# Performance work log

Measured on AMD Instinct MI355X. Metric: run time of the kernel, lower is better.

Reference implementation:

```python
import math
import jax, jax.numpy as jnp
import numpy as np

THETA = 10000.0

def _rotate_half(x):
    # lucidrains interleaved pairs: (d r) with r=2
    x = x.reshape(*x.shape[:-1], -1, 2)
    x1, x2 = x[..., 0], x[..., 1]
    return jnp.stack([-x2, x1], axis=-1).reshape(*x.shape[:-2], -1)

def _apply_rotary(x):
    # x: [B, H, S, D]
    seq_len, d = x.shape[-2], x.shape[-1]
    inv_freq = 1.0 / (THETA ** (jnp.arange(0, d, 2, dtype=jnp.float32) / d))  # [D/2]
    t = jnp.arange(seq_len, dtype=jnp.float32)
    freqs = t[:, None] * inv_freq[None, :]                 # [S, D/2]
    freqs = jnp.repeat(freqs, 2, axis=-1)                  # [S, D] interleaved
    cos, sin = jnp.cos(freqs), jnp.sin(freqs)
    return x * cos + _rotate_half(x) * sin

def setup_inputs() -> dict:
    key = jax.random.key(0)
    k1, k2, k3, k4 = jax.random.split(key, 4)
    B, H, S, D = 2, 16, 2048, 64
    q = jax.random.normal(k1, (B, H, S, D), dtype=jnp.float32)
    k = jax.random.normal(k2, (B, H, S, D), dtype=jnp.float32)
    v = jax.random.normal(k3, (B, H, S, D), dtype=jnp.float32)
    mask = jax.random.randint(k4, (B, 1, S, S), 0, 2, dtype=jnp.int32)
    return {"q": q, "k": k, "v": v, "mask": mask}

def reference(q, k, v, mask):
    d = k.shape[-1]
    qr = _apply_rotary(q)
    kr = _apply_rotary(k)
    score = jnp.einsum('bhqd,bhkd->bhqk', qr, kr) / math.sqrt(d)
    score = jnp.where(mask == 0, jnp.float32(-10000.0), score)
    score = jax.nn.softmax(score, axis=-1)
    out = jnp.einsum('bhqk,bhkd->bhqd', score, v)
    return (out, score)
```

## Files before the change

### kernel.cpp

```cpp
#include <hip/hip_runtime.h>
#include <hip/hip_fp16.h>

#define NB 2
#define NH 16
#define NS 2048
#define ND 64

typedef __attribute__((ext_vector_type(8))) _Float16 half8;
typedef __attribute__((ext_vector_type(4))) _Float16 half4;
typedef __attribute__((ext_vector_type(4))) float float4v;

static constexpr int NE = NB * NH * NS * ND;
static constexpr int TPB = 512;

__device__ __forceinline__ void wg_barrier_lds() {
    asm volatile("s_waitcnt lgkmcnt(0)" ::: "memory");
    __builtin_amdgcn_s_barrier();
    __builtin_amdgcn_sched_barrier(0);
}

static constexpr int ROPE_BLKS = (NE / 2) / 256;
static constexpr int VT_BLKS   = NE / 256;
static constexpr int MP_BLKS   = (NB * NS * NS) / 256;

__global__ void prep_kernel(const float* __restrict__ q,
                            const float* __restrict__ k,
                            const float* __restrict__ v,
                            const int* __restrict__ mask,
                            _Float16* __restrict__ qr,
                            _Float16* __restrict__ kr6,
                            _Float16* __restrict__ v4,
                            unsigned int* __restrict__ mp) {
    int blk = blockIdx.x;
    if (blk < ROPE_BLKS) {
        int idx = blk * 256 + threadIdx.x;
        int i   = idx & 31;
        int row = idx >> 5;
        int s   = row & (NS - 1);
        int bh  = row >> 11;

        float inv_freq = expf((float)i * -0.2878231366242710f);
        float ang = (float)s * inv_freq;
        float sn, cs;
        sincosf(ang, &sn, &cs);

        size_t base = (size_t)row * ND + 2 * i;
        float q0 = q[base], q1 = q[base + 1];
        float k0 = k[base], k1 = k[base + 1];
        qr[base]     = (_Float16)(q0 * cs - q1 * sn);
        qr[base + 1] = (_Float16)(q1 * cs + q0 * sn);

        int oct = i >> 2;
        int j0  = (2 * i) & 7;
        size_t t6 = ((size_t)(bh * 128 + (s >> 4)) * 8 + oct) * 128 + (s & 15) * 8 + j0;
        kr6[t6]     = (_Float16)(k0 * cs - k1 * sn);
        kr6[t6 + 1] = (_Float16)(k1 * cs + k0 * sn);
    } else if (blk < ROPE_BLKS + VT_BLKS) {
        int idx = (blk - ROPE_BLKS) * 256 + threadIdx.x;
        int j    = idx & 3;
        int lm   = (idx >> 2) & 15;
        int kq   = (idx >> 6) & 3;
        int dblk = (idx >> 8) & 3;
        int kt   = (idx >> 10) & 127;
        int bh   = idx >> 17;
        int key  = kt * 16 + kq * 4 + j;
        int d    = dblk * 16 + lm;
        v4[idx] = (_Float16)v[((size_t)bh * NS + key) * ND + d];
    } else {
        size_t idx = (size_t)(blk - ROPE_BLKS - VT_BLKS) * 256 + threadIdx.x;
        unsigned long long bal = __ballot(mask[idx] != 0);
        int l = threadIdx.x & 63;
        if (l == 0)       mp[idx >> 5] = (unsigned int)bal;
        else if (l == 32) mp[idx >> 5] = (unsigned int)(bal >> 32);
    }
}

static constexpr int TPH    = 264;
static constexpr int WSLICE = 16 * TPH;

__global__ __launch_bounds__(TPB, 4)
void attn_reg_kernel(const _Float16* __restrict__ qr,
                     const _Float16* __restrict__ kr6,
                     const _Float16* __restrict__ v4,
                     const unsigned int* __restrict__ mp,
                     float* __restrict__ out,
                     float* __restrict__ score) {
    __shared__ unsigned int maskb[16 * 64];
    __shared__ float        sums8[8][16];
    __shared__ _Float16     pool[8 * WSLICE];

    int wgid = (blockIdx.x & 7) * 512 + (blockIdx.x >> 3);
    int qt = wgid & 127;
    int bh = wgid >> 7;
    int b  = bh >> 4;
    int q0 = qt * 16;

    int tid = threadIdx.x;
    int w   = tid >> 6;
    int l   = tid & 63;
    int lm  = l & 15;
    int lp  = l >> 4;

    {
        const unsigned int* mrow = mp + ((size_t)b * NS + q0) * 64;
        for (int i = tid; i < 16 * 64; i += TPB) maskb[i] = mrow[i];
    }

    const _Float16* qrow = qr + ((size_t)bh * NS + q0 + lm) * ND;
    half8 a0 = *(const half8*)(qrow + lp * 8);
    half8 a1 = *(const half8*)(qrow + 32 + lp * 8);
    const _Float16* k6 = kr6 + (size_t)bh * 128 * 1024;
    _Float16* tw = pool + w * WSLICE;
    wg_barrier_lds();

    float4v ac0 = {0.f, 0.f, 0.f, 0.f};
    float4v ac1 = {0.f, 0.f, 0.f, 0.f};
    float4v ac2 = {0.f, 0.f, 0.f, 0.f};
    float4v ac3 = {0.f, 0.f, 0.f, 0.f};
    const _Float16* vb = v4 + (size_t)bh * 128 * 1024 + l * 4;
    float ps = 0.0f;
#pragma unroll
    for (int t = 0; t < 16; ++t) {
        int kt = w * 16 + t;
        const _Float16* kp = k6 + (size_t)kt * 1024 + l * 8;
        half8 b0 = *(const half8*)(kp);
        half8 b1 = *(const half8*)(kp + 512);
        float4v acc = {0.f, 0.f, 0.f, 0.f};
        acc = __builtin_amdgcn_mfma_f32_16x16x32_f16(b0, a0, acc, 0, 0, 0);
        acc = __builtin_amdgcn_mfma_f32_16x16x32_f16(b1, a1, acc, 0, 0, 0);
        int keyb = kt * 16 + lp * 4;
        unsigned int mw = maskb[lm * 64 + (keyb >> 5)];
        int bit0 = keyb & 31;
        half4 ep;
#pragma unroll
        for (int r = 0; r < 4; ++r) {
            float ev = ((mw >> (bit0 + r)) & 1u) ? __expf(acc[r] * 0.125f) : 0.0f;
            ps += ev;
            ep[r] = (_Float16)ev;
        }
        *(half4*)(tw + lm * TPH + t * 16 + lp * 4) = ep;

        const _Float16* vp = vb + (size_t)kt * 1024;
        half4 af0 = *(const half4*)(vp);
        half4 af1 = *(const half4*)(vp + 256);
        half4 af2 = *(const half4*)(vp + 512);
        half4 af3 = *(const half4*)(vp + 768);
        __builtin_amdgcn_s_setprio(1);
        ac0 = __builtin_amdgcn_mfma_f32_16x16x16f16(af0, ep, ac0, 0, 0, 0);
        ac1 = __builtin_amdgcn_mfma_f32_16x16x16f16(af1, ep, ac1, 0, 0, 0);
        ac2 = __builtin_amdgcn_mfma_f32_16x16x16f16(af2, ep, ac2, 0, 0, 0);
        ac3 = __builtin_amdgcn_mfma_f32_16x16x16f16(af3, ep, ac3, 0, 0, 0);
        __builtin_amdgcn_s_setprio(0);
    }
    ps += __shfl_xor(ps, 16);
    ps += __shfl_xor(ps, 32);
    if (lp == 0) sums8[w][lm] = ps;
    wg_barrier_lds();

    {
        float s = 0.0f;
#pragma unroll
        for (int ww = 0; ww < 8; ++ww) s += sums8[ww][lm];
        float iv = (s > 0.0f) ? (1.0f / s) : 0.0f;
        float* sbase = score + ((size_t)bh * NS + q0) * NS + w * 256;
#pragma unroll
        for (int r = 0; r < 16; ++r) {
            float ivr = __shfl(iv, r);
            half4 hv = *(const half4*)(tw + r * TPH + l * 4);
            float4v f;
            f[0] = (float)hv[0] * ivr;
            f[1] = (float)hv[1] * ivr;
            f[2] = (float)hv[2] * ivr;
            f[3] = (float)hv[3] * ivr;
            *(float4v*)(sbase + (size_t)r * NS + l * 4) = f;
        }
    }
    asm volatile("s_waitcnt lgkmcnt(0)" ::: "memory");
    __builtin_amdgcn_sched_barrier(0);

    {
        float* ow = (float*)tw + lm * 64 + lp * 4;
#pragma unroll
        for (int r = 0; r < 4; ++r) {
            ow[ 0 + r] = ac0[r];
            ow[16 + r] = ac1[r];
            ow[32 + r] = ac2[r];
            ow[48 + r] = ac3[r];
        }
    }
    wg_barrier_lds();

    {
        float* orow = out + ((size_t)bh * NS + q0) * ND;
        for (int i = tid; i < 16 * 64; i += TPB) {
            int r = i >> 6;
            float s = 0.0f;
#pragma unroll
            for (int ww = 0; ww < 8; ++ww) s += sums8[ww][r];
            float iv = (s > 0.0f) ? (1.0f / s) : 0.0f;
            float acc = 0.0f;
#pragma unroll
            for (int ww = 0; ww < 8; ++ww)
                acc += ((const float*)(pool + ww * WSLICE))[i];
            __builtin_nontemporal_store(acc * iv, &orow[i]);
        }
    }
}

extern "C" void kernel_launch(void* const* d_in, const int* in_sizes, int n_in,
                              void* d_out, int out_size, void* d_ws, size_t ws_size,
                              hipStream_t stream) {
    const float* q    = (const float*)d_in[0];
    const float* k    = (const float*)d_in[1];
    const float* v    = (const float*)d_in[2];
    const int*   mask = (const int*)d_in[3];

    float* out   = (float*)d_out;
    float* score = out + (size_t)NE;

    _Float16* qrw = (_Float16*)d_ws;
    _Float16* kr6 = qrw + NE;
    _Float16* v4w = kr6 + NE;
    unsigned int* mp = (unsigned int*)(v4w + NE);

    prep_kernel<<<dim3(ROPE_BLKS + VT_BLKS + MP_BLKS), dim3(256), 0, stream>>>(
        q, k, v, mask, qrw, kr6, v4w, mp);
    attn_reg_kernel<<<dim3(NB * NH * (NS / 16)), dim3(TPB), 0, stream>>>(
        qrw, kr6, v4w, mp, out, score);
}
```

Measured before the change: 208.7 us.

## Halve per-wave LDS staging by holding half the P tile in registers

Each wave now stages only the first 8 key tiles of exp-scores in LDS, and keeps the last 8 in registers. The score output is written in two passes: the second half is copied back into the freed LDS slice before it is normalised and stored. This halves the LDS pool so more workgroups can fit per CU, and the launch bound is raised from 4 to 6 to match. Score writes also switch to nontemporal float2 stores. The risks are extra VGPR pressure from the held tiles under the tighter register budget, which could spill, and narrower stores to global memory.

```diff
diff --git a/kernel.cpp b/kernel.cpp
--- a/kernel.cpp
+++ b/kernel.cpp
@@ -9,13 +9,18 @@
 typedef __attribute__((ext_vector_type(8))) _Float16 half8;
 typedef __attribute__((ext_vector_type(4))) _Float16 half4;
 typedef __attribute__((ext_vector_type(4))) float float4v;
-
-static constexpr int NE = NB * NH * NS * ND;
+typedef __attribute__((ext_vector_type(2))) float float2v;
+
+static constexpr int NE  = NB * NH * NS * ND;
 static constexpr int TPB = 512;
 
 __device__ __forceinline__ void wg_barrier_lds() {
     asm volatile("s_waitcnt lgkmcnt(0)" ::: "memory");
     __builtin_amdgcn_s_barrier();
+    __builtin_amdgcn_sched_barrier(0);
+}
+__device__ __forceinline__ void wave_lds_guard() {
+    asm volatile("s_waitcnt lgkmcnt(0)" ::: "memory");
     __builtin_amdgcn_sched_barrier(0);
 }
 
@@ -75,10 +80,10 @@
     }
 }
 
-static constexpr int TPH    = 264;
+static constexpr int TPH    = 136;
 static constexpr int WSLICE = 16 * TPH;
 
-__global__ __launch_bounds__(TPB, 4)
+__global__ __launch_bounds__(TPB, 6)
 void attn_reg_kernel(const _Float16* __restrict__ qr,
                      const _Float16* __restrict__ kr6,
                      const _Float16* __restrict__ v4,
@@ -110,6 +115,7 @@
     half8 a0 = *(const half8*)(qrow + lp * 8);
     half8 a1 = *(const half8*)(qrow + 32 + lp * 8);
     const _Float16* k6 = kr6 + (size_t)bh * 128 * 1024;
+    const _Float16* vb = v4 + (size_t)bh * 128 * 1024 + l * 4;
     _Float16* tw = pool + w * WSLICE;
     wg_barrier_lds();
 
@@ -117,7 +123,7 @@
     float4v ac1 = {0.f, 0.f, 0.f, 0.f};
     float4v ac2 = {0.f, 0.f, 0.f, 0.f};
     float4v ac3 = {0.f, 0.f, 0.f, 0.f};
-    const _Float16* vb = v4 + (size_t)bh * 128 * 1024 + l * 4;
+    half4 earr[8];
     float ps = 0.0f;
 #pragma unroll
     for (int t = 0; t < 16; ++t) {
@@ -138,8 +144,11 @@
             ps += ev;
             ep[r] = (_Float16)ev;
         }
-        *(half4*)(tw + lm * TPH + t * 16 + lp * 4) = ep;
-
+        if (t < 8) {
+            *(half4*)(tw + lm * TPH + t * 16 + lp * 4) = ep;
+        } else {
+            earr[t - 8] = ep;
+        }
         const _Float16* vp = vb + (size_t)kt * 1024;
         half4 af0 = *(const half4*)(vp);
         half4 af1 = *(const half4*)(vp + 256);
@@ -163,21 +172,34 @@
         for (int ww = 0; ww < 8; ++ww) s += sums8[ww][lm];
         float iv = (s > 0.0f) ? (1.0f / s) : 0.0f;
         float* sbase = score + ((size_t)bh * NS + q0) * NS + w * 256;
+
 #pragma unroll
         for (int r = 0; r < 16; ++r) {
             float ivr = __shfl(iv, r);
-            half4 hv = *(const half4*)(tw + r * TPH + l * 4);
-            float4v f;
-            f[0] = (float)hv[0] * ivr;
-            f[1] = (float)hv[1] * ivr;
-            f[2] = (float)hv[2] * ivr;
-            f[3] = (float)hv[3] * ivr;
-            *(float4v*)(sbase + (size_t)r * NS + l * 4) = f;
-        }
-    }
-    asm volatile("s_waitcnt lgkmcnt(0)" ::: "memory");
-    __builtin_amdgcn_sched_barrier(0);
-
+            half res0 = tw[r * TPH + l * 2];
+            half res1 = tw[r * TPH + l * 2 + 1];
+            float2v f;
+            f[0] = (float)(_Float16)res0 * ivr;
+            f[1] = (float)(_Float16)res1 * ivr;
+            __builtin_nontemporal_store(f, (float2v*)(sbase + (size_t)r * NS + l * 2));
+        }
+        wave_lds_guard();
+#pragma unroll
+        for (int t = 0; t < 8; ++t)
+            *(half4*)(tw + lm * TPH + t * 16 + lp * 4) = earr[t];
+        wave_lds_guard();
+#pragma unroll
+        for (int r = 0; r < 16; ++r) {
+            float ivr = __shfl(iv, r);
+            half res0 = tw[r * TPH + l * 2];
+            half res1 = tw[r * TPH + l * 2 + 1];
+            float2v f;
+            f[0] = (float)(_Float16)res0 * ivr;
+            f[1] = (float)(_Float16)res1 * ivr;
+            __builtin_nontemporal_store(f, (float2v*)(sbase + (size_t)r * NS + 128 + l * 2));
+        }
+    }
+    wave_lds_guard();
     {
         float* ow = (float*)tw + lm * 64 + lp * 4;
 #pragma unroll
```

Result: slower. 281.2 us (+34.8%).
